# Optimization experiments

Measured on AMD Instinct MI355X. Metric: run time of the kernel, lower is better.

The kernel has to match this reference:

```python
import jax, jax.numpy as jnp
import numpy as np

D_MODEL = 1024
NUM_HEADS = 16
GROUPS = 4
HEADS_PER_GROUP = NUM_HEADS // GROUPS
D_K = D_MODEL // NUM_HEADS
B, S = 2, 2048


def setup_inputs() -> dict:
    key = jax.random.key(0)
    ks = jax.random.split(key, 10)
    sc = 0.02
    return {
        "x": jax.random.normal(ks[0], (B, S, D_MODEL), dtype=jnp.float32),
        "W_Q": jax.random.normal(ks[1], (D_MODEL, D_MODEL), dtype=jnp.float32) * sc,
        "b_Q": jnp.zeros((D_MODEL,), dtype=jnp.float32),
        "W_K": jax.random.normal(ks[2], (GROUPS, D_MODEL, D_K), dtype=jnp.float32) * sc,
        "b_K": jnp.zeros((GROUPS, D_K), dtype=jnp.float32),
        "W_V": jax.random.normal(ks[3], (GROUPS, D_MODEL, D_K), dtype=jnp.float32) * sc,
        "b_V": jnp.zeros((GROUPS, D_K), dtype=jnp.float32),
        "W_O": jax.random.normal(ks[4], (D_MODEL, D_MODEL), dtype=jnp.float32) * sc,
        "b_O": jnp.zeros((D_MODEL,), dtype=jnp.float32),
    }


def reference(x, W_Q, b_Q, W_K, b_K, W_V, b_V, W_O, b_O):
    b, s, _ = x.shape
    # Q: [b, s, d_model] -> [b, groups, heads_per_group, s, d_k]
    Q = (x @ W_Q + b_Q).reshape(b, s, NUM_HEADS, D_K).transpose(0, 2, 1, 3)
    Q = Q.reshape(b, GROUPS, HEADS_PER_GROUP, s, D_K)
    # Shared K/V per group: [b, groups, s, d_k]
    K = jnp.einsum('bsd,gdk->bgsk', x, W_K) + b_K[None, :, None, :]
    V = jnp.einsum('bsd,gdk->bgsk', x, W_V) + b_V[None, :, None, :]
    # scores: [b, groups, heads_per_group, s, s]
    scores = jnp.einsum('bghsk,bgtk->bghst', Q, K) / jnp.sqrt(jnp.float32(D_K))
    attn = jax.nn.softmax(scores, axis=-1)
    # context: [b, groups, heads_per_group, s, d_k] -> [b, s, d_model]
    ctx = jnp.einsum('bghst,bgtk->bghsk', attn, V)
    ctx = ctx.reshape(b, NUM_HEADS, s, D_K).transpose(0, 2, 1, 3).reshape(b, s, D_MODEL)
    return ctx @ W_O + b_O
```

## Files before the change

### kernel.cpp

```cpp
#include <hip/hip_runtime.h>
#include <cstdint>
#include <cstddef>

typedef short bf16x8 __attribute__((ext_vector_type(8)));
typedef float f32x4 __attribute__((ext_vector_type(4)));

#define DM 1024
#define NHEADS 16
#define NGROUPS 4
#define DK 64
#define BATCH 2
#define SEQ 2048
#define MROWS 4096

#define QB_ELEMS   ((size_t)BATCH*NHEADS*SEQ*DK)
#define KB_ELEMS   ((size_t)BATCH*NGROUPS*SEQ*DK)
#define VT_ELEMS   KB_ELEMS
#define XC_ELEMS   ((size_t)MROWS*DM)
#define WQKV_ELEMS ((size_t)1536*DM)
#define WO_ELEMS   ((size_t)DM*DM)

#define SCL_Q 0.180336880f

__device__ __forceinline__ ushort f2bf(float f) {
    union { float f; uint32_t u; } a; a.f = f;
    uint32_t u = a.u;
    return (ushort)((u + 0x7FFFu + ((u >> 16) & 1u)) >> 16);
}

__device__ __forceinline__ void gll16(const void* g, void* l) {
    __builtin_amdgcn_global_load_lds((const __attribute__((address_space(1))) void*)g,
                                     (__attribute__((address_space(3))) void*)l, 16, 0, 0);
}

__device__ __forceinline__ void transpose_tile(
        const float* __restrict__ src, int src_ld, ushort* __restrict__ dst,
        int r0, int c0, int tid, float (*tl)[65])
{
    const int rr = tid >> 4, cc = (tid & 15) * 4;
#pragma unroll
    for (int p = 0; p < 4; p++) {
        int r = rr + p * 16;
        float4 v = *(const float4*)(src + (size_t)(r0 + r) * src_ld + c0 + cc);
        tl[cc + 0][r] = v.x; tl[cc + 1][r] = v.y;
        tl[cc + 2][r] = v.z; tl[cc + 3][r] = v.w;
    }
    __syncthreads();
#pragma unroll
    for (int p = 0; p < 4; p++) {
        int c = rr + p * 16;
        ushort4 o;
        o.x = f2bf(tl[c][cc + 0]); o.y = f2bf(tl[c][cc + 1]);
        o.z = f2bf(tl[c][cc + 2]); o.w = f2bf(tl[c][cc + 3]);
        *(ushort4*)(dst + (size_t)(c0 + c) * 1024 + r0 + cc) = o;
    }
}

__global__ __launch_bounds__(256) void gqa_prep_kernel(
        const float* __restrict__ x,
        const float* __restrict__ WQ, const float* __restrict__ WK,
        const float* __restrict__ WV,
        const float* __restrict__ bQ, const float* __restrict__ bK,
        const float* __restrict__ bV,
        ushort* __restrict__ xbf, ushort* __restrict__ WqkvT,
        float* __restrict__ bcat)
{
    __shared__ float tl[64][65];
    const int bid = blockIdx.x, tid = threadIdx.x;
    if (bid < 256) {
        transpose_tile(WQ, 1024, WqkvT, (bid >> 4) * 64, (bid & 15) * 64, tid, tl);
    } else if (bid < 320) {
        int t = bid - 256, g = t >> 4;
        transpose_tile(WK + (size_t)g * 1024 * 64, 64,
                       WqkvT + (size_t)(1024 + g * 64) * 1024,
                       (t & 15) * 64, 0, tid, tl);
    } else if (bid < 384) {
        int t = bid - 320, g = t >> 4;
        transpose_tile(WV + (size_t)g * 1024 * 64, 64,
                       WqkvT + (size_t)(1280 + g * 64) * 1024,
                       (t & 15) * 64, 0, tid, tl);
    } else if (bid < 640) {
        int cid = bid - 384;
        const float* xs = x + (size_t)cid * 16384;
        ushort* xd = xbf + (size_t)cid * 16384;
#pragma unroll
        for (int p = 0; p < 16; p++) {
            float4 v = *(const float4*)(xs + p * 1024 + tid * 4);
            ushort4 o = { f2bf(v.x), f2bf(v.y), f2bf(v.z), f2bf(v.w) };
            *(ushort4*)(xd + p * 1024 + tid * 4) = o;
        }
    } else {
        for (int i = tid; i < 1536; i += 256) {
            float v = (i < 1024) ? bQ[i] : (i < 1280 ? bK[i - 1024] : bV[i - 1280]);
            bcat[i] = v;
        }
    }
}

template<bool QKV_EPI, int BN, bool RIDERS>
__global__ __launch_bounds__(256, 2) void gqa_gemm_kernel(
        const ushort* __restrict__ A, const ushort* __restrict__ BT,
        const float* __restrict__ bias, float* __restrict__ outF,
        ushort* __restrict__ Qb, ushort* __restrict__ Kb, ushort* __restrict__ Vtg,
        const float* __restrict__ WO, ushort* __restrict__ WoT)
{
    __shared__ ushort smem[4][8192];
    const int tid = threadIdx.x;
    int i = blockIdx.x;

    if constexpr (RIDERS) {
        if (i < 256) {
            float (*tl)[65] = (float(*)[65])&smem[0][0];
            transpose_tile(WO, 1024, WoT, (i >> 4) * 64, (i & 15) * 64, tid, tl);
            return;
        }
        i -= 256;
    }

    const int xcd = i & 7, slot = i >> 3;
    const int bm = (slot / BN) * 8 + xcd;
    const int bn = slot % BN;
    const int wave = tid >> 6, lane = tid & 63;
    const int wm = (wave & 1) * 64, wn = (wave >> 1) * 64;
    const int lr = lane & 15, lq = lane >> 4;
    const int swz = lr & 7;

    const ushort* srcA[4]; const ushort* srcB[4]; int dstOff[4];
#pragma unroll
    for (int p = 0; p < 4; p++) {
        int slt = p * 256 + tid;
        int row = slt >> 3, cb = (slt & 7) ^ (row & 7);
        srcA[p] = A  + (size_t)(bm * 128 + row) * 1024 + cb * 8;
        srcB[p] = BT + (size_t)(bn * 128 + row) * 1024 + cb * 8;
        dstOff[p] = p * 2048 + wave * 512;
    }

    f32x4 acc[4][4];
#pragma unroll
    for (int ii = 0; ii < 4; ii++)
#pragma unroll
        for (int j = 0; j < 4; j++) acc[ii][j] = (f32x4){0.f, 0.f, 0.f, 0.f};

#pragma unroll
    for (int p = 0; p < 4; p++) {
        gll16(srcA[p], &smem[0][dstOff[p]]);
        gll16(srcB[p], &smem[2][dstOff[p]]);
    }

    for (int kt = 0; kt < 16; kt++) {
        __syncthreads();
        if (kt < 15) {
            int buf = (kt + 1) & 1, ko = (kt + 1) * 64;
#pragma unroll
            for (int p = 0; p < 4; p++) {
                gll16(srcA[p] + ko, &smem[buf][dstOff[p]]);
                gll16(srcB[p] + ko, &smem[2 + buf][dstOff[p]]);
            }
        }
        const ushort* as = smem[kt & 1];
        const ushort* bs = smem[2 + (kt & 1)];
        bf16x8 af[2][4], bfr[2][4];
#pragma unroll
        for (int kh = 0; kh < 2; kh++) {
#pragma unroll
            for (int ii = 0; ii < 4; ii++)
                af[kh][ii] = *(const bf16x8*)&as[(wm + ii * 16 + lr) * 64 + ((kh * 4 + lq) ^ swz) * 8];
#pragma unroll
            for (int j = 0; j < 4; j++)
                bfr[kh][j] = *(const bf16x8*)&bs[(wn + j * 16 + lr) * 64 + ((kh * 4 + lq) ^ swz) * 8];
        }
#pragma unroll
        for (int kh = 0; kh < 2; kh++)
#pragma unroll
            for (int ii = 0; ii < 4; ii++)
#pragma unroll
                for (int j = 0; j < 4; j++)
                    acc[ii][j] = __builtin_amdgcn_mfma_f32_16x16x32_bf16(af[kh][ii], bfr[kh][j], acc[ii][j], 0, 0, 0);
    }

#pragma unroll
    for (int ii = 0; ii < 4; ii++) {
        int mg = bm * 128 + wm + ii * 16 + lq * 4;
        int b = mg >> 11, s = mg & 2047;
#pragma unroll
        for (int j = 0; j < 4; j++) {
            int cg = bn * 128 + wn + j * 16 + lr;
            float bv = bias[cg];
            if constexpr (QKV_EPI) {
                int d = cg & 63;
                if (cg < 1024) {
                    int h = cg >> 6;
                    ushort* dst = Qb + ((size_t)(b * NHEADS + h) * SEQ + s) * DK + d;
#pragma unroll
                    for (int r = 0; r < 4; r++)
                        dst[r * DK] = f2bf((acc[ii][j][r] + bv) * SCL_Q);
                } else if (cg < 1280) {
                    int g = (cg - 1024) >> 6;
                    ushort* dst = Kb + ((size_t)(b * NGROUPS + g) * SEQ + s) * DK + d;
#pragma unroll
                    for (int r = 0; r < 4; r++) dst[r * DK] = f2bf(acc[ii][j][r] + bv);
                } else {
                    int g = (cg - 1280) >> 6;
                    int s4 = s >> 2, kg = s4 & 7;
                    int col = ((s4 >> 3) << 5) + (((((kg & 3) << 1) | (kg >> 2))) << 2);
                    ushort4 pk;
                    pk.x = f2bf(acc[ii][j][0] + bv); pk.y = f2bf(acc[ii][j][1] + bv);
                    pk.z = f2bf(acc[ii][j][2] + bv); pk.w = f2bf(acc[ii][j][3] + bv);
                    *(ushort4*)(Vtg + ((size_t)(b * NGROUPS + g) * DK + d) * SEQ + col) = pk;
                }
            } else {
#pragma unroll
                for (int r = 0; r < 4; r++)
                    outF[(size_t)(mg + r) * DM + cg] = acc[ii][j][r] + bv;
            }
        }
    }
}

__global__ __launch_bounds__(256, 2) void gqa_attn_kernel(
        const ushort* __restrict__ Qb, const ushort* __restrict__ Kb,
        const ushort* __restrict__ Vtg, ushort* __restrict__ ctx)
{
    __shared__ ushort Ks[2][128 * 64];
    __shared__ ushort Vs[2][64 * 128];

    const int tid = threadIdx.x, wave = tid >> 6, lane = tid & 63;
    const int lr = lane & 15, lq = lane >> 4;
    const int swz = lr & 7;
    const int wq = wave & 1, wt = wave >> 1;
    const int i = blockIdx.x;
    const int bg = i & 7, s2 = i >> 3;
    const int qt = s2 & 15, h = s2 >> 4;
    const int b = bg >> 2, g = bg & 3, hg = g * 4 + h;

    const ushort* Qh = Qb  + (size_t)(b * NHEADS  + hg) * SEQ * DK;
    const ushort* Kg = Kb  + (size_t)(b * NGROUPS + g)  * SEQ * DK;
    const ushort* Vg = Vtg + (size_t)(b * NGROUPS + g)  * DK * SEQ;

    const int s0 = qt * 128 + wq * 64;
    const int tb = wt * 64;

    bf16x8 qf[4][2];
#pragma unroll
    for (int qs = 0; qs < 4; qs++)
#pragma unroll
        for (int kh = 0; kh < 2; kh++)
            qf[qs][kh] = *(const bf16x8*)(Qh + (size_t)(s0 + qs * 16 + lr) * DK + kh * 32 + lq * 8);

    const ushort* srcK[4]; const ushort* srcV[4]; int dstOff[4];
#pragma unroll
    for (int p = 0; p < 4; p++) {
        int slt = p * 256 + tid;
        int krow = slt >> 3, kcb = (slt & 7) ^ (krow & 7);
        srcK[p] = Kg + (size_t)krow * DK + kcb * 8;
        int vrow = slt >> 4, vc = slt & 15;
        int vcb = (vc & 8) | ((vc ^ vrow) & 7);
        srcV[p] = Vg + (size_t)vrow * SEQ + vcb * 8;
        dstOff[p] = (p * 256 + wave * 64) * 8;
    }

    f32x4 of[4][4];
#pragma unroll
    for (int qs = 0; qs < 4; qs++)
#pragma unroll
        for (int j = 0; j < 4; j++) of[qs][j] = (f32x4){0.f, 0.f, 0.f, 0.f};
    f32x4 accL[4];
#pragma unroll
    for (int qs = 0; qs < 4; qs++) accL[qs] = (f32x4){0.f, 0.f, 0.f, 0.f};

    bf16x8 ones;
#pragma unroll
    for (int k = 0; k < 8; k++) ones[k] = (short)0x3F80;

#pragma unroll
    for (int p = 0; p < 4; p++) {
        gll16(srcK[p], &Ks[0][dstOff[p]]);
        gll16(srcV[p], &Vs[0][dstOff[p]]);
    }

    for (int it = 0; it < 16; it++) {
        __syncthreads();
        if (it < 15) {
            int buf = (it + 1) & 1, t0 = (it + 1) * 128;
#pragma unroll
            for (int p = 0; p < 4; p++) {
                gll16(srcK[p] + (size_t)t0 * DK, &Ks[buf][dstOff[p]]);
                gll16(srcV[p] + t0, &Vs[buf][dstOff[p]]);
            }
        }
        const ushort* ks = Ks[it & 1];
        const ushort* vs = Vs[it & 1];

        bf16x8 kf[4][2];
#pragma unroll
        for (int nt = 0; nt < 4; nt++)
#pragma unroll
            for (int kh = 0; kh < 2; kh++)
                kf[nt][kh] = *(const bf16x8*)&ks[(tb + nt * 16 + lr) * 64 + ((kh * 4 + lq) ^ swz) * 8];

        bf16x8 vf[4][2];
#pragma unroll
        for (int j = 0; j < 4; j++)
#pragma unroll
            for (int kk = 0; kk < 2; kk++)
                vf[j][kk] = *(const bf16x8*)&vs[(j * 16 + lr) * 128 + (wt * 8 + ((kk * 4 + lq) ^ swz)) * 8];

        f32x4 sc[4][4];
#pragma unroll
        for (int qs = 0; qs < 4; qs++)
#pragma unroll
            for (int nt = 0; nt < 4; nt++) {
                f32x4 s = (f32x4){0.f, 0.f, 0.f, 0.f};
                s = __builtin_amdgcn_mfma_f32_16x16x32_bf16(kf[nt][0], qf[qs][0], s, 0, 0, 0);
                s = __builtin_amdgcn_mfma_f32_16x16x32_bf16(kf[nt][1], qf[qs][1], s, 0, 0, 0);
                sc[qs][nt] = s;
            }

        union PF { bf16x8 v; uint32_t w[4]; };
        PF pf[4][2];
#pragma unroll
        for (int qs = 0; qs < 4; qs++) {
#pragma unroll
            for (int nt = 0; nt < 4; nt++) {
                union { float f; uint32_t u; } e0, e1, e2, e3;
                e0.f = __builtin_amdgcn_exp2f(sc[qs][nt][0]);
                e1.f = __builtin_amdgcn_exp2f(sc[qs][nt][1]);
                e2.f = __builtin_amdgcn_exp2f(sc[qs][nt][2]);
                e3.f = __builtin_amdgcn_exp2f(sc[qs][nt][3]);
                pf[qs][nt >> 1].w[(nt & 1) * 2 + 0] = __builtin_amdgcn_perm(e1.u, e0.u, 0x07060302u);
                pf[qs][nt >> 1].w[(nt & 1) * 2 + 1] = __builtin_amdgcn_perm(e3.u, e2.u, 0x07060302u);
            }
            accL[qs] = __builtin_amdgcn_mfma_f32_16x16x32_bf16(ones, pf[qs][0].v, accL[qs], 0, 0, 0);
            accL[qs] = __builtin_amdgcn_mfma_f32_16x16x32_bf16(ones, pf[qs][1].v, accL[qs], 0, 0, 0);
        }

#pragma unroll
        for (int qs = 0; qs < 4; qs++)
#pragma unroll
            for (int j = 0; j < 4; j++) {
                of[qs][j] = __builtin_amdgcn_mfma_f32_16x16x32_bf16(vf[j][0], pf[qs][0].v, of[qs][j], 0, 0, 0);
                of[qs][j] = __builtin_amdgcn_mfma_f32_16x16x32_bf16(vf[j][1], pf[qs][1].v, of[qs][j], 0, 0, 0);
            }
    }

    __syncthreads();
    float* comb = (float*)&Ks[0][0];
    float* accX = (float*)&Vs[0][0];
    if (wt == 1) {
        float* cw = comb + wq * 4096;
#pragma unroll
        for (int qs = 0; qs < 4; qs++)
#pragma unroll
            for (int j = 0; j < 4; j++)
                *(f32x4*)&cw[(qs * 4 + j) * 256 + lane * 4] = of[qs][j];
        if (lq == 0) {
#pragma unroll
            for (int qs = 0; qs < 4; qs++) accX[(wq * 4 + qs) * 16 + lr] = accL[qs][0];
        }
    }
    __syncthreads();
    if (wt == 0) {
        const float* cw = comb + wq * 4096;
        float inv[4];
#pragma unroll
        for (int qs = 0; qs < 4; qs++)
            inv[qs] = 1.0f / (accL[qs][0] + accX[(wq * 4 + qs) * 16 + lr]);
        ushort* cbp = ctx + (size_t)b * SEQ * DM;
#pragma unroll
        for (int qs = 0; qs < 4; qs++) {
            int s = s0 + qs * 16 + lr;
#pragma unroll
            for (int j = 0; j < 4; j++) {
                f32x4 o2 = of[qs][j] + *(const f32x4*)&cw[(qs * 4 + j) * 256 + lane * 4];
                ushort4 o;
                o.x = f2bf(o2[0] * inv[qs]);
                o.y = f2bf(o2[1] * inv[qs]);
                o.z = f2bf(o2[2] * inv[qs]);
                o.w = f2bf(o2[3] * inv[qs]);
                *(ushort4*)(cbp + (size_t)s * DM + hg * 64 + j * 16 + lq * 4) = o;
            }
        }
    }
}

extern "C" void kernel_launch(void* const* d_in, const int* in_sizes, int n_in,
                              void* d_out, int out_size, void* d_ws, size_t ws_size,
                              hipStream_t stream) {
    const float* x  = (const float*)d_in[0];
    const float* WQ = (const float*)d_in[1];
    const float* bQ = (const float*)d_in[2];
    const float* WK = (const float*)d_in[3];
    const float* bK = (const float*)d_in[4];
    const float* WV = (const float*)d_in[5];
    const float* bV = (const float*)d_in[6];
    const float* WO = (const float*)d_in[7];
    const float* bO = (const float*)d_in[8];

    ushort* Qb    = (ushort*)d_ws;
    ushort* Kb    = Qb + QB_ELEMS;
    ushort* Vtg   = Kb + KB_ELEMS;
    ushort* xc    = Vtg + VT_ELEMS;
    ushort* WqkvT = xc + XC_ELEMS;
    ushort* WoT   = WqkvT + WQKV_ELEMS;
    float*  bcat  = (float*)(WoT + WO_ELEMS);

    gqa_prep_kernel<<<641, 256, 0, stream>>>(x, WQ, WK, WV, bQ, bK, bV,
                                             xc, WqkvT, bcat);
    gqa_gemm_kernel<true, 12, true><<<640, 256, 0, stream>>>(
        xc, WqkvT, bcat, nullptr, Qb, Kb, Vtg, WO, WoT);
    gqa_attn_kernel<<<512, 256, 0, stream>>>(Qb, Kb, Vtg, xc);
    gqa_gemm_kernel<false, 8, false><<<256, 256, 0, stream>>>(
        xc, WoT, bO, (float*)d_out, nullptr, nullptr, nullptr, nullptr, nullptr);
}
```

Measured before the change: 156.7 us.

## Move WO transpose into prep kernel and retile GEMMs to 512 blocks

The WO weight transpose moves out of the QKV GEMM launch, where it rode along as extra blocks, and into the prep kernel. The prep kernel now runs a grid-stride loop of 512 blocks over 897 work units. Both GEMMs become templated on the N-tile width: 96 columns for QKV and 64 for the output projection, each launched as 512 blocks so the grid maps evenly onto the CUs. This aims at better load balance and no tail wave, at the cost of smaller N tiles with less A-tile reuse and more A-matrix traffic.

New measurement: 161.4 us. 1.03x slower.

```diff
diff --git a/kernel.cpp b/kernel.cpp
--- a/kernel.cpp
+++ b/kernel.cpp
@@ -59,114 +59,121 @@
 __global__ __launch_bounds__(256) void gqa_prep_kernel(
         const float* __restrict__ x,
         const float* __restrict__ WQ, const float* __restrict__ WK,
-        const float* __restrict__ WV,
+        const float* __restrict__ WV, const float* __restrict__ WO,
         const float* __restrict__ bQ, const float* __restrict__ bK,
         const float* __restrict__ bV,
         ushort* __restrict__ xbf, ushort* __restrict__ WqkvT,
-        float* __restrict__ bcat)
+        ushort* __restrict__ WoT, float* __restrict__ bcat)
 {
     __shared__ float tl[64][65];
-    const int bid = blockIdx.x, tid = threadIdx.x;
-    if (bid < 256) {
-        transpose_tile(WQ, 1024, WqkvT, (bid >> 4) * 64, (bid & 15) * 64, tid, tl);
-    } else if (bid < 320) {
-        int t = bid - 256, g = t >> 4;
-        transpose_tile(WK + (size_t)g * 1024 * 64, 64,
-                       WqkvT + (size_t)(1024 + g * 64) * 1024,
-                       (t & 15) * 64, 0, tid, tl);
-    } else if (bid < 384) {
-        int t = bid - 320, g = t >> 4;
-        transpose_tile(WV + (size_t)g * 1024 * 64, 64,
-                       WqkvT + (size_t)(1280 + g * 64) * 1024,
-                       (t & 15) * 64, 0, tid, tl);
-    } else if (bid < 640) {
-        int cid = bid - 384;
-        const float* xs = x + (size_t)cid * 16384;
-        ushort* xd = xbf + (size_t)cid * 16384;
-#pragma unroll
-        for (int p = 0; p < 16; p++) {
-            float4 v = *(const float4*)(xs + p * 1024 + tid * 4);
-            ushort4 o = { f2bf(v.x), f2bf(v.y), f2bf(v.z), f2bf(v.w) };
-            *(ushort4*)(xd + p * 1024 + tid * 4) = o;
-        }
-    } else {
-        for (int i = tid; i < 1536; i += 256) {
-            float v = (i < 1024) ? bQ[i] : (i < 1280 ? bK[i - 1024] : bV[i - 1280]);
-            bcat[i] = v;
-        }
-    }
-}
-
-template<bool QKV_EPI, int BN, bool RIDERS>
+    const int tid = threadIdx.x;
+    for (int u = blockIdx.x; u < 897; u += 512) {
+        if (u < 256) {
+            transpose_tile(WQ, 1024, WqkvT, (u >> 4) * 64, (u & 15) * 64, tid, tl);
+        } else if (u < 320) {
+            int t = u - 256, g = t >> 4;
+            transpose_tile(WK + (size_t)g * 65536, 64,
+                           WqkvT + (size_t)(1024 + g * 64) * 1024,
+                           (t & 15) * 64, 0, tid, tl);
+        } else if (u < 384) {
+            int t = u - 320, g = t >> 4;
+            transpose_tile(WV + (size_t)g * 65536, 64,
+                           WqkvT + (size_t)(1280 + g * 64) * 1024,
+                           (t & 15) * 64, 0, tid, tl);
+        } else if (u < 640) {
+            int t = u - 384;
+            transpose_tile(WO, 1024, WoT, (t >> 4) * 64, (t & 15) * 64, tid, tl);
+        } else if (u < 896) {
+            int cid = u - 640;
+            const float* xs = x + (size_t)cid * 16384;
+            ushort* xd = xbf + (size_t)cid * 16384;
+#pragma unroll
+            for (int p = 0; p < 16; p++) {
+                float4 v = *(const float4*)(xs + p * 1024 + tid * 4);
+                ushort4 o = { f2bf(v.x), f2bf(v.y), f2bf(v.z), f2bf(v.w) };
+                *(ushort4*)(xd + p * 1024 + tid * 4) = o;
+            }
+        } else {
+            for (int k = tid; k < 1536; k += 256) {
+                float v = (k < 1024) ? bQ[k] : (k < 1280 ? bK[k - 1024] : bV[k - 1280]);
+                bcat[k] = v;
+            }
+        }
+        __syncthreads();
+    }
+}
+
+template<int NJ, bool QKV_EPI>
 __global__ __launch_bounds__(256, 2) void gqa_gemm_kernel(
         const ushort* __restrict__ A, const ushort* __restrict__ BT,
         const float* __restrict__ bias, float* __restrict__ outF,
-        ushort* __restrict__ Qb, ushort* __restrict__ Kb, ushort* __restrict__ Vtg,
-        const float* __restrict__ WO, ushort* __restrict__ WoT)
+        ushort* __restrict__ Qb, ushort* __restrict__ Kb,
+        ushort* __restrict__ Vtg)
 {
-    __shared__ ushort smem[4][8192];
+    constexpr int BNT = NJ * 32;
+    __shared__ ushort smem[16384 + NJ * 4096];
+    ushort* As = smem;
+    ushort* Bs = smem + 16384;
+
     const int tid = threadIdx.x;
-    int i = blockIdx.x;
-
-    if constexpr (RIDERS) {
-        if (i < 256) {
-            float (*tl)[65] = (float(*)[65])&smem[0][0];
-            transpose_tile(WO, 1024, WoT, (i >> 4) * 64, (i & 15) * 64, tid, tl);
-            return;
-        }
-        i -= 256;
-    }
-
+    const int i = blockIdx.x;
     const int xcd = i & 7, slot = i >> 3;
-    const int bm = (slot / BN) * 8 + xcd;
-    const int bn = slot % BN;
+    const int bm = (slot >> 4) * 8 + xcd;
+    const int bn = slot & 15;
     const int wave = tid >> 6, lane = tid & 63;
-    const int wm = (wave & 1) * 64, wn = (wave >> 1) * 64;
+    const int wm = (wave & 1) * 64, wn = (wave >> 1) * (NJ * 16);
     const int lr = lane & 15, lq = lane >> 4;
     const int swz = lr & 7;
 
-    const ushort* srcA[4]; const ushort* srcB[4]; int dstOff[4];
+    const ushort* srcA[4]; int dstOffA[4];
+    const ushort* srcB[NJ]; int dstOffB[NJ];
 #pragma unroll
     for (int p = 0; p < 4; p++) {
         int slt = p * 256 + tid;
         int row = slt >> 3, cb = (slt & 7) ^ (row & 7);
-        srcA[p] = A  + (size_t)(bm * 128 + row) * 1024 + cb * 8;
-        srcB[p] = BT + (size_t)(bn * 128 + row) * 1024 + cb * 8;
-        dstOff[p] = p * 2048 + wave * 512;
-    }
-
-    f32x4 acc[4][4];
+        srcA[p] = A + (size_t)(bm * 128 + row) * 1024 + cb * 8;
+        dstOffA[p] = p * 2048 + wave * 512;
+    }
+#pragma unroll
+    for (int p = 0; p < NJ; p++) {
+        int slt = p * 256 + tid;
+        int row = slt >> 3, cb = (slt & 7) ^ (row & 7);
+        srcB[p] = BT + (size_t)(bn * BNT + row) * 1024 + cb * 8;
+        dstOffB[p] = p * 2048 + wave * 512;
+    }
+
+    f32x4 acc[4][NJ];
 #pragma unroll
     for (int ii = 0; ii < 4; ii++)
 #pragma unroll
-        for (int j = 0; j < 4; j++) acc[ii][j] = (f32x4){0.f, 0.f, 0.f, 0.f};
-
-#pragma unroll
-    for (int p = 0; p < 4; p++) {
-        gll16(srcA[p], &smem[0][dstOff[p]]);
-        gll16(srcB[p], &smem[2][dstOff[p]]);
-    }
+        for (int j = 0; j < NJ; j++) acc[ii][j] = (f32x4){0.f, 0.f, 0.f, 0.f};
+
+#pragma unroll
+    for (int p = 0; p < 4; p++) gll16(srcA[p], &As[dstOffA[p]]);
+#pragma unroll
+    for (int p = 0; p < NJ; p++) gll16(srcB[p], &Bs[dstOffB[p]]);
 
     for (int kt = 0; kt < 16; kt++) {
         __syncthreads();
         if (kt < 15) {
             int buf = (kt + 1) & 1, ko = (kt + 1) * 64;
 #pragma unroll
-            for (int p = 0; p < 4; p++) {
-                gll16(srcA[p] + ko, &smem[buf][dstOff[p]]);
-                gll16(srcB[p] + ko, &smem[2 + buf][dstOff[p]]);
-            }
-        }
-        const ushort* as = smem[kt & 1];
-        const ushort* bs = smem[2 + (kt & 1)];
-        bf16x8 af[2][4], bfr[2][4];
+            for (int p = 0; p < 4; p++)
+                gll16(srcA[p] + ko, &As[buf * 8192 + dstOffA[p]]);
+#pragma unroll
+            for (int p = 0; p < NJ; p++)
+                gll16(srcB[p] + ko, &Bs[buf * (NJ * 2048) + dstOffB[p]]);
+        }
+        const ushort* as = As + (kt & 1) * 8192;
+        const ushort* bs = Bs + (kt & 1) * (NJ * 2048);
+        bf16x8 af[2][4], bfr[2][NJ];
 #pragma unroll
         for (int kh = 0; kh < 2; kh++) {
 #pragma unroll
             for (int ii = 0; ii < 4; ii++)
                 af[kh][ii] = *(const bf16x8*)&as[(wm + ii * 16 + lr) * 64 + ((kh * 4 + lq) ^ swz) * 8];
 #pragma unroll
-            for (int j = 0; j < 4; j++)
+            for (int j = 0; j < NJ; j++)
                 bfr[kh][j] = *(const bf16x8*)&bs[(wn + j * 16 + lr) * 64 + ((kh * 4 + lq) ^ swz) * 8];
         }
 #pragma unroll
@@ -174,7 +181,7 @@
 #pragma unroll
             for (int ii = 0; ii < 4; ii++)
 #pragma unroll
-                for (int j = 0; j < 4; j++)
+                for (int j = 0; j < NJ; j++)
                     acc[ii][j] = __builtin_amdgcn_mfma_f32_16x16x32_bf16(af[kh][ii], bfr[kh][j], acc[ii][j], 0, 0, 0);
     }
 
@@ -183,8 +190,8 @@
         int mg = bm * 128 + wm + ii * 16 + lq * 4;
         int b = mg >> 11, s = mg & 2047;
 #pragma unroll
-        for (int j = 0; j < 4; j++) {
-            int cg = bn * 128 + wn + j * 16 + lr;
+        for (int j = 0; j < NJ; j++) {
+            int cg = bn * BNT + wn + j * 16 + lr;
             float bv = bias[cg];
             if constexpr (QKV_EPI) {
                 int d = cg & 63;
@@ -404,11 +411,11 @@
     ushort* WoT   = WqkvT + WQKV_ELEMS;
     float*  bcat  = (float*)(WoT + WO_ELEMS);
 
-    gqa_prep_kernel<<<641, 256, 0, stream>>>(x, WQ, WK, WV, bQ, bK, bV,
-                                             xc, WqkvT, bcat);
-    gqa_gemm_kernel<true, 12, true><<<640, 256, 0, stream>>>(
-        xc, WqkvT, bcat, nullptr, Qb, Kb, Vtg, WO, WoT);
+    gqa_prep_kernel<<<512, 256, 0, stream>>>(x, WQ, WK, WV, WO, bQ, bK, bV,
+                                             xc, WqkvT, WoT, bcat);
+    gqa_gemm_kernel<3, true><<<512, 256, 0, stream>>>(
+        xc, WqkvT, bcat, nullptr, Qb, Kb, Vtg);
     gqa_attn_kernel<<<512, 256, 0, stream>>>(Qb, Kb, Vtg, xc);
-    gqa_gemm_kernel<false, 8, false><<<256, 256, 0, stream>>>(
-        xc, WoT, bO, (float*)d_out, nullptr, nullptr, nullptr, nullptr, nullptr);
-}
+    gqa_gemm_kernel<2, false><<<512, 256, 0, stream>>>(
+        xc, WoT, bO, (float*)d_out, nullptr, nullptr, nullptr);
+}
```
